# Performance work log

Measured on AMD Instinct MI355X. Metric: run time of the kernel, lower is better.

The kernel has to match this reference:

```python
import jax, jax.numpy as jnp
import numpy as np

B, T, E, D = 8, 2048, 1024, 128  # batch, seq, embedding_dim, head_dim


def setup_inputs() -> dict:
    key = jax.random.key(0)
    ks = jax.random.split(key, 7)
    s = 1.0 / np.sqrt(E)  # torch Linear default init scale
    return {
        "x": jax.random.normal(ks[0], (B, T, E), dtype=jnp.float32),
        "Wq": jax.random.uniform(ks[1], (E, D), jnp.float32, -s, s),
        "bq": jax.random.uniform(ks[2], (D,), jnp.float32, -s, s),
        "Wk": jax.random.uniform(ks[3], (E, D), jnp.float32, -s, s),
        "bk": jax.random.uniform(ks[4], (D,), jnp.float32, -s, s),
        "Wv": jax.random.uniform(ks[5], (E, D), jnp.float32, -s, s),
        "bv": jax.random.uniform(ks[6], (D,), jnp.float32, -s, s),
        "mask": 1,
    }


def reference(x, Wq, bq, Wk, bk, Wv, bv, mask):
    # Q/K/V projections: [B,T,E] @ [E,D] -> [B,T,D]
    q = x @ Wq + bq
    k = x @ Wk + bk
    v = x @ Wv + bv
    d_k = q.shape[-1]
    # scores: [B,T,T]
    scores = jnp.einsum("btd,bsd->bts", q, k) / jnp.sqrt(jnp.float32(d_k))
    if mask:  # causal masked_fill with -inf (static python flag)
        causal = jnp.tril(jnp.ones((q.shape[1], q.shape[1]), dtype=bool))
        scores = jnp.where(causal[None, :, :], scores, -jnp.inf)
    att = jax.nn.softmax(scores, axis=-1)
    # dropout p=0.0 (inference) -> identity
    return jnp.einsum("bts,bsd->btd", att, v)
```

## Files before the change

kernel.cpp:

```cpp
#include <hip/hip_runtime.h>
#include <hip/hip_bf16.h>

#define BSZ  8
#define TSEQ 2048
#define EDIM 1024
#define DDIM 128
#define MROWS (BSZ * TSEQ)
#define NQT  (TSEQ / 64)

typedef __attribute__((ext_vector_type(8))) __bf16 bf16x8;
typedef __attribute__((ext_vector_type(4))) __bf16 bf16x4;
typedef __attribute__((ext_vector_type(2))) __bf16 bf16x2;
typedef __attribute__((ext_vector_type(4))) float f32x4;

#define GLOAD_LDS(G, L) \
    __builtin_amdgcn_global_load_lds( \
        (const __attribute__((address_space(1))) void*)(G), \
        (__attribute__((address_space(3))) void*)(L), 16, 0, 0)

__global__ __launch_bounds__(256) void wt_kernel(
    const float* __restrict__ Wq, const float* __restrict__ Wk,
    const float* __restrict__ Wv, __bf16* __restrict__ wt)
{
    const float* W = (blockIdx.y == 0) ? Wq : (blockIdx.y == 1) ? Wk : Wv;
    __bf16* o = wt + (size_t)blockIdx.y * DDIM * EDIM;
    const int k0 = blockIdx.x * 64;
    __shared__ __align__(16) __bf16 t[64][140];
    const int tid = threadIdx.x;
    #pragma unroll
    for (int i = 0; i < 8; ++i) {
        int idx = tid + i * 256;
        int k = idx >> 5, c4 = idx & 31;
        float4 v = *(const float4*)&W[(size_t)(k0 + k) * DDIM + c4 * 4];
        bf16x4 b4;
        b4[0] = (__bf16)v.x; b4[1] = (__bf16)v.y; b4[2] = (__bf16)v.z; b4[3] = (__bf16)v.w;
        *(bf16x4*)&t[k][c4 * 4] = b4;
    }
    __syncthreads();
    #pragma unroll
    for (int i = 0; i < 4; ++i) {
        int idx = tid + i * 256;
        int n = idx >> 3, c8 = idx & 7;
        bf16x8 r;
        #pragma unroll
        for (int u = 0; u < 8; ++u) r[u] = t[c8 * 8 + u][n];
        *(bf16x8*)&o[(size_t)n * EDIM + k0 + c8 * 8] = r;
    }
}

#define A_LDS_BYTES 16384
#define B_LDS_BYTES 24576
#define BUF_BYTES   (A_LDS_BYTES + B_LDS_BYTES)

__global__ __launch_bounds__(256, 2) void qkv_fused_kernel(
    const float* __restrict__ x, const __bf16* __restrict__ wt,
    const float* __restrict__ bq, const float* __restrict__ bk,
    const float* __restrict__ bv,
    __bf16* __restrict__ qo, __bf16* __restrict__ ko, __bf16* __restrict__ vto)
{
    const int bid = blockIdx.x;
    const int xcd = bid & 7;
    const int nt  = (bid >> 3) & 1;
    const int mt  = (bid >> 4) * 8 + xcd;
    const int m0  = mt * 64;

    __shared__ __align__(16) char lds[2 * BUF_BYTES];

    const int tid  = threadIdx.x;
    const int lane = tid & 63;
    const int wv   = tid >> 6;
    const int wr   = wv >> 1, wc = wv & 1;
    const int cl   = lane & 15, gr = lane >> 4;

    f32x4 acc[2][6] = {};

    const float* asrc[4];
    int adst[4];
    #pragma unroll
    for (int i = 0; i < 4; ++i) {
        const int row  = i * 16 + (tid >> 4);
        const int lcol = ((tid & 15) * 16) ^ ((row & 7) << 4);
        asrc[i] = x + (size_t)(m0 + row) * EDIM + (lcol >> 2);
        adst[i] = i * 4096 + tid * 16;
    }
    const __bf16* bsrc[6];
    int bdst[6];
    #pragma unroll
    for (int i = 0; i < 6; ++i) {
        const int row  = i * 32 + (tid >> 3);
        const int lcol = ((tid & 7) * 16) ^ ((row & 7) << 4);
        bsrc[i] = wt + (size_t)(nt * 192 + row) * EDIM + (lcol >> 1);
        bdst[i] = A_LDS_BYTES + i * 4096 + tid * 16;
    }

    const int sw = (cl & 7) << 4;

#define STAGE(BUF, K0) do {                                                   \
    _Pragma("unroll")                                                         \
    for (int i = 0; i < 4; ++i)                                               \
        GLOAD_LDS(asrc[i] + (K0), lds + (BUF) * BUF_BYTES + adst[i]);         \
    _Pragma("unroll")                                                         \
    for (int i = 0; i < 6; ++i)                                               \
        GLOAD_LDS(bsrc[i] + (K0), lds + (BUF) * BUF_BYTES + bdst[i]);         \
  } while (0)

#define COMPUTE(BUF) do {                                                     \
    const char* base_ = lds + (BUF) * BUF_BYTES;                              \
    _Pragma("unroll")                                                         \
    for (int ks = 0; ks < 2; ++ks) {                                          \
        bf16x8 af[2], bfr[6];                                                 \
        _Pragma("unroll")                                                     \
        for (int mi = 0; mi < 2; ++mi) {                                      \
            const int ab = (wr * 32 + mi * 16 + cl) * 256 + ks * 128;         \
            f32x4 lo = *(const f32x4*)(base_ + ab + ((gr * 32)      ^ sw));   \
            f32x4 hi = *(const f32x4*)(base_ + ab + ((gr * 32 + 16) ^ sw));   \
            bf16x8 t;                                                         \
            t[0] = (__bf16)lo[0]; t[1] = (__bf16)lo[1];                       \
            t[2] = (__bf16)lo[2]; t[3] = (__bf16)lo[3];                       \
            t[4] = (__bf16)hi[0]; t[5] = (__bf16)hi[1];                       \
            t[6] = (__bf16)hi[2]; t[7] = (__bf16)hi[3];                       \
            af[mi] = t;                                                       \
        }                                                                     \
        _Pragma("unroll")                                                     \
        for (int ni = 0; ni < 6; ++ni) {                                      \
            const int off = A_LDS_BYTES + (wc * 96 + ni * 16 + cl) * 128      \
                          + ((ks * 64 + gr * 16) ^ sw);                       \
            bfr[ni] = *(const bf16x8*)(base_ + off);                          \
        }                                                                     \
        _Pragma("unroll")                                                     \
        for (int mi = 0; mi < 2; ++mi)                                        \
            _Pragma("unroll")                                                 \
            for (int ni = 0; ni < 6; ++ni)                                    \
                acc[mi][ni] = __builtin_amdgcn_mfma_f32_16x16x32_bf16(        \
                    af[mi], bfr[ni], acc[mi][ni], 0, 0, 0);                   \
    }                                                                         \
  } while (0)

    STAGE(0, 0);
    __syncthreads();

    #pragma unroll 1
    for (int k0 = 0; k0 < EDIM; k0 += 128) {
        STAGE(1, k0 + 64);
        COMPUTE(0);
        __syncthreads();
        if (k0 + 128 < EDIM) STAGE(0, k0 + 128);
        COMPUTE(1);
        __syncthreads();
    }
#undef STAGE
#undef COMPUTE

    const float qsc = 0.08838834764831845f;
    #pragma unroll
    for (int ni = 0; ni < 6; ++ni) {
        const int nbase = nt * 192 + wc * 96 + ni * 16;
        const int which = nbase >> 7;
        const int d     = (nbase & 127) + cl;
        const float* bias = (which == 0) ? bq : (which == 1) ? bk : bv;
        const float bb = bias[d];
        const float sc = (which == 0) ? qsc : 1.0f;
        #pragma unroll
        for (int mi = 0; mi < 2; ++mi) {
            const int row = m0 + wr * 32 + mi * 16 + gr * 4;
            if (which == 2) {
                bf16x4 p;
                #pragma unroll
                for (int r = 0; r < 4; ++r) p[r] = (__bf16)(acc[mi][ni][r] + bb);
                *(bf16x4*)&vto[(size_t)d * MROWS + row] = p;
            } else {
                __bf16* o = (which == 0) ? qo : ko;
                #pragma unroll
                for (int r = 0; r < 4; ++r)
                    o[(size_t)(row + r) * DDIM + d] = (__bf16)((acc[mi][ni][r] + bb) * sc);
            }
        }
    }
}

__global__ __launch_bounds__(256, 3) void attn_partial_kernel(
    const __bf16* __restrict__ Q, const __bf16* __restrict__ K,
    const __bf16* __restrict__ Vt,
    __bf16* __restrict__ partO, float* __restrict__ partM, float* __restrict__ partL,
    int PL, int NP)
{
    const int bid = blockIdx.x;
    const int b   = blockIdx.y;

    int g = 0, rem = bid;
    for (;;) {
        const int np_g = (g + 1 + PL - 1) / PL;
        if (rem < np_g) break;
        rem -= np_g; ++g;
    }
    const int qt = g, p = rem;
    const int tiles = qt + 1;
    const int np = (tiles + PL - 1) / PL;
    const int lb = tiles / np, ex = tiles % np;
    const int mylen = lb + (p < ex);
    const int start = p * lb + min(p, ex);
    const int kv_lo = start * 64;
    const int kv_hi = kv_lo + mylen * 64;

    __shared__ __align__(16) __bf16 k_l[64 * 128];
    __shared__ __align__(16) __bf16 v_l[128 * 64];
    __shared__ __align__(16) __bf16 p_l[4][16 * 64];

    const int tid  = threadIdx.x;
    const int lane = tid & 63;
    const int w    = tid >> 6;
    const int cl   = lane & 15, gr = lane >> 4;
    const int ek   = (cl & 7) * 8;

    const int qrow = qt * 64 + w * 16;
    const size_t bT = (size_t)b * TSEQ;

    bf16x8 qf[4];
    const __bf16* qbase = Q + (bT + qrow + cl) * DDIM;
    #pragma unroll
    for (int ks = 0; ks < 4; ++ks)
        qf[ks] = *(const bf16x8*)&qbase[ks * 32 + gr * 8];

    f32x4 acc[8] = {};
    float m1 = -__builtin_inff();
    float l1 = 0.f;

    bf16x8 rk[4], rv[4];
#define LOAD_TILE(KV0) do {                                                   \
    _Pragma("unroll")                                                         \
    for (int i = 0; i < 4; ++i) {                                             \
        int idx = tid + i * 256;                                              \
        rk[i] = *(const bf16x8*)&K[(bT + (KV0) + (idx >> 4)) * DDIM + (idx & 15) * 8]; } \
    _Pragma("unroll")                                                         \
    for (int i = 0; i < 4; ++i) {                                             \
        int idx = tid + i * 256;                                              \
        rv[i] = *(const bf16x8*)&Vt[(size_t)(idx >> 3) * MROWS + bT + (KV0) + (idx & 7) * 8]; } \
  } while (0)

    LOAD_TILE(kv_lo);

    #pragma unroll 1
    for (int kv0 = kv_lo; kv0 < kv_hi; kv0 += 64) {
        #pragma unroll
        for (int i = 0; i < 4; ++i) {
            int idx = tid + i * 256;
            int row = idx >> 4;
            *(bf16x8*)&k_l[row * 128 + (((idx & 15) * 8) ^ ((row & 7) * 8))] = rk[i];
        }
        #pragma unroll
        for (int i = 0; i < 4; ++i) {
            int idx = tid + i * 256;
            int row = idx >> 3;
            *(bf16x8*)&v_l[row * 64 + (((idx & 7) * 8) ^ ((row & 7) * 8))] = rv[i];
        }
        __syncthreads();

        if (kv0 + 64 < kv_hi) LOAD_TILE(kv0 + 64);

        f32x4 s[4] = {};
        __builtin_amdgcn_s_setprio(1);
        #pragma unroll
        for (int ks = 0; ks < 4; ++ks) {
            #pragma unroll
            for (int st = 0; st < 4; ++st) {
                bf16x8 kf = *(const bf16x8*)&k_l[(st * 16 + cl) * 128
                                                 + ((ks * 32 + gr * 8) ^ ek)];
                s[st] = __builtin_amdgcn_mfma_f32_16x16x32_bf16(kf, qf[ks], s[st], 0, 0, 0);
            }
        }
        __builtin_amdgcn_s_setprio(0);

        if (kv0 + 63 > qrow) {
            const int kvb = kv0 + gr * 4 - qrow - cl;
            #pragma unroll
            for (int st = 0; st < 4; ++st)
                #pragma unroll
                for (int r = 0; r < 4; ++r)
                    if (kvb + st * 16 + r > 0) s[st][r] = -__builtin_inff();
        }

        float tm = fmaxf(fmaxf(fmaxf(s[0][0], s[0][1]), fmaxf(s[0][2], s[0][3])),
                         fmaxf(fmaxf(s[1][0], s[1][1]), fmaxf(s[1][2], s[1][3])));
        tm = fmaxf(tm,
             fmaxf(fmaxf(fmaxf(s[2][0], s[2][1]), fmaxf(s[2][2], s[2][3])),
                   fmaxf(fmaxf(s[3][0], s[3][1]), fmaxf(s[3][2], s[3][3]))));
        tm = fmaxf(tm, __shfl_xor(tm, 16));
        tm = fmaxf(tm, __shfl_xor(tm, 32));

        if (__any(tm > m1)) {
            const float newm = fmaxf(m1, tm);
            const float alpha = __expf(m1 - newm);
            l1 *= alpha;
            m1 = newm;
            float arec[4];
            #pragma unroll
            for (int r = 0; r < 4; ++r) arec[r] = __shfl(alpha, gr * 4 + r);
            #pragma unroll
            for (int d = 0; d < 8; ++d) {
                #pragma unroll
                for (int r = 0; r < 4; ++r) acc[d][r] *= arec[r];
            }
        }

        #pragma unroll
        for (int st = 0; st < 4; ++st) {
            #pragma unroll
            for (int u = 0; u < 2; ++u) {
                float p0 = __expf(s[st][2 * u]     - m1);
                float p1 = __expf(s[st][2 * u + 1] - m1);
                l1 += p0 + p1;
                bf16x2 pp; pp[0] = (__bf16)p0; pp[1] = (__bf16)p1;
                *(bf16x2*)&p_l[w][cl * 64 + ((st * 16 + gr * 4 + 2 * u) ^ ek)] = pp;
            }
        }

        __builtin_amdgcn_s_setprio(1);
        #pragma unroll
        for (int ks2 = 0; ks2 < 2; ++ks2) {
            bf16x8 pa = *(const bf16x8*)&p_l[w][cl * 64 + ((ks2 * 32 + gr * 8) ^ ek)];
            #pragma unroll
            for (int d = 0; d < 8; ++d) {
                bf16x8 vf = *(const bf16x8*)&v_l[(d * 16 + cl) * 64
                                                 + ((ks2 * 32 + gr * 8) ^ ek)];
                acc[d] = __builtin_amdgcn_mfma_f32_16x16x32_bf16(pa, vf, acc[d], 0, 0, 0);
            }
        }
        __builtin_amdgcn_s_setprio(0);
        __syncthreads();
    }
#undef LOAD_TILE

    const size_t pidx = (size_t)b * NP + bid;
    __bf16* po = partO + pidx * (64 * 128);
    float ls = l1;
    ls += __shfl_xor(ls, 16);
    ls += __shfl_xor(ls, 32);
    if (gr == 0) {
        partM[pidx * 64 + w * 16 + cl] = m1;
        partL[pidx * 64 + w * 16 + cl] = ls;
    }
    #pragma unroll
    for (int r = 0; r < 4; ++r) {
        const int row_l = w * 16 + gr * 4 + r;
        #pragma unroll
        for (int d = 0; d < 8; ++d)
            po[row_l * 128 + d * 16 + cl] = (__bf16)acc[d][r];
    }
}

__global__ __launch_bounds__(256) void attn_combine_kernel(
    const __bf16* __restrict__ partO, const float* __restrict__ partM,
    const float* __restrict__ partL, float* __restrict__ out, int PL, int NP)
{
    const int qt = blockIdx.x, b = blockIdx.y;
    int pre = 0;
    for (int g2 = 0; g2 < qt; ++g2) pre += (g2 + 1 + PL - 1) / PL;
    const int nv = (qt + 1 + PL - 1) / PL;
    const size_t pbase = (size_t)b * NP + pre;

    const int tid = threadIdx.x;
    const int col = (tid & 31) * 4;
    const int rbase = blockIdx.z * 32;

    #pragma unroll
    for (int rr = 0; rr < 4; ++rr) {
        const int row = rbase + (tid >> 5) + rr * 8;
        float mx = -__builtin_inff();
        for (int c = 0; c < nv; ++c)
            mx = fmaxf(mx, partM[(pbase + c) * 64 + row]);
        float lsum = 0.f;
        f32x4 o = {0.f, 0.f, 0.f, 0.f};
        for (int c = 0; c < nv; ++c) {
            const float wgt = __expf(partM[(pbase + c) * 64 + row] - mx);
            lsum += wgt * partL[(pbase + c) * 64 + row];
            const bf16x4 po = *(const bf16x4*)&partO[(pbase + c) * (64 * 128) + (size_t)row * 128 + col];
            o.x += wgt * (float)po[0]; o.y += wgt * (float)po[1];
            o.z += wgt * (float)po[2]; o.w += wgt * (float)po[3];
        }
        const float inv = 1.0f / lsum;
        f32x4 res = {o.x * inv, o.y * inv, o.z * inv, o.w * inv};
        *(f32x4*)&out[((size_t)b * TSEQ + qt * 64 + row) * DDIM + col] = res;
    }
}

extern "C" void kernel_launch(void* const* d_in, const int* in_sizes, int n_in,
                              void* d_out, int out_size, void* d_ws, size_t ws_size,
                              hipStream_t stream) {
    const float* x  = (const float*)d_in[0];
    const float* Wq = (const float*)d_in[1];
    const float* bq = (const float*)d_in[2];
    const float* Wk = (const float*)d_in[3];
    const float* bk = (const float*)d_in[4];
    const float* Wv = (const float*)d_in[5];
    const float* bv = (const float*)d_in[6];

    __bf16* q  = (__bf16*)d_ws;
    __bf16* k  = q  + (size_t)MROWS * DDIM;
    __bf16* vt = k  + (size_t)MROWS * DDIM;
    __bf16* wt = vt + (size_t)MROWS * DDIM;
    const size_t fixed_bytes = ((size_t)3 * MROWS * DDIM + (size_t)3 * DDIM * EDIM) * sizeof(__bf16);

    int PL = 4, NP = 0;
    for (int g2 = 0; g2 < NQT; ++g2) NP += (g2 + 1 + PL - 1) / PL;
    {
        const size_t need = fixed_bytes +
            (size_t)NP * BSZ * 64 * (128 * sizeof(__bf16) + 2 * sizeof(float));
        if (ws_size < need) {
            PL = 8; NP = 0;
            for (int g2 = 0; g2 < NQT; ++g2) NP += (g2 + 1 + PL - 1) / PL;
        }
    }
    __bf16* partO = (__bf16*)((char*)d_ws + fixed_bytes);
    float* partM = (float*)(partO + (size_t)NP * BSZ * 64 * 128);
    float* partL = partM + (size_t)NP * BSZ * 64;

    wt_kernel<<<dim3(EDIM / 64, 3), 256, 0, stream>>>(Wq, Wk, Wv, wt);
    qkv_fused_kernel<<<dim3(MROWS / 64 * 2), 256, 0, stream>>>(x, wt, bq, bk, bv, q, k, vt);
    attn_partial_kernel<<<dim3(NP, BSZ), 256, 0, stream>>>(q, k, vt, partO, partM, partL, PL, NP);
    attn_combine_kernel<<<dim3(NQT, BSZ, 2), 256, 0, stream>>>(partO, partM, partL,
                                                               (float*)d_out, PL, NP);
}
```

Before: 78.24 us.

## Keep two stages in flight in QKV projection GEMM with partial vmcnt waits

Restructures the projection GEMM's double-buffered K loop so both LDS stages are prefetched up front. It replaces the full __syncthreads waits with raw s_barrier plus s_waitcnt vmcnt(10), so only the older stage must land before compute while the newer load stays outstanding. This aims to overlap global-to-LDS loads with MFMA compute more deeply. It relies on the exact count of outstanding load instructions per stage, which is fragile if STAGE's instruction count changes.

Result: no change. 79.75 us (+1.9%).

```diff
diff --git a/kernel.cpp b/kernel.cpp
--- a/kernel.cpp
+++ b/kernel.cpp
@@ -137,16 +137,36 @@
   } while (0)
 
     STAGE(0, 0);
-    __syncthreads();
+    STAGE(1, 64);
+    asm volatile("s_waitcnt vmcnt(10)" ::: "memory");
+    __builtin_amdgcn_sched_barrier(0);
+    __builtin_amdgcn_s_barrier();
 
     #pragma unroll 1
-    for (int k0 = 0; k0 < EDIM; k0 += 128) {
-        STAGE(1, k0 + 64);
+    for (int t = 0; t < 16; t += 2) {
         COMPUTE(0);
-        __syncthreads();
-        if (k0 + 128 < EDIM) STAGE(0, k0 + 128);
+        __builtin_amdgcn_s_barrier();
+        if (t + 2 < 16) {
+            STAGE(0, (t + 2) * 64);
+            asm volatile("s_waitcnt vmcnt(10)" ::: "memory");
+        } else {
+            asm volatile("s_waitcnt vmcnt(0)" ::: "memory");
+        }
+        __builtin_amdgcn_sched_barrier(0);
+        __builtin_amdgcn_s_barrier();
+
         COMPUTE(1);
-        __syncthreads();
+        if (t + 2 < 16) {
+            __builtin_amdgcn_s_barrier();
+            if (t + 3 < 16) {
+                STAGE(1, (t + 3) * 64);
+                asm volatile("s_waitcnt vmcnt(10)" ::: "memory");
+            } else {
+                asm volatile("s_waitcnt vmcnt(0)" ::: "memory");
+            }
+            __builtin_amdgcn_sched_barrier(0);
+            __builtin_amdgcn_s_barrier();
+        }
     }
 #undef STAGE
 #undef COMPUTE
```
